# Optimization experiments

Measured on AMD Instinct MI355X. Metric: run time of the kernel, lower is better.

The kernel has to match this reference:

```python
import jax, jax.numpy as jnp
import numpy as np

N = 50000
E = 800000
EQ = 200000
IN_DIM = 256
H1 = 256
H2 = 128
EA = 16


def _lrelu(x):
    return jax.nn.leaky_relu(x, negative_slope=0.01)


def gcn_conv(h, edge_index, W, b, num_nodes):
    # PyG GCNConv: add self-loops, symmetric normalization, out = A_hat (h W) + b
    row, col = edge_index[0], edge_index[1]
    loop = jnp.arange(num_nodes, dtype=row.dtype)
    row = jnp.concatenate([row, loop])
    col = jnp.concatenate([col, loop])
    deg = jax.ops.segment_sum(jnp.ones(row.shape[0], dtype=h.dtype), col, num_segments=num_nodes)
    dinv = jnp.where(deg > 0, jax.lax.rsqrt(deg), 0.0)
    norm = dinv[row] * dinv[col]                      # [E+N]
    hw = h @ W                                        # [N, out]
    msg = hw[row] * norm[:, None]                     # gather + scale
    out = jax.ops.segment_sum(msg, col, num_segments=num_nodes)
    return out + b


def gru_cell(x, h, Wih, Whh, bih, bhh):
    # torch.nn.GRUCell, gate order (r, z, n); Wih/Whh stored as [in, 3H]
    gi = x @ Wih + bih
    gh = h @ Whh + bhh
    ir, iz, inn = jnp.split(gi, 3, axis=1)
    hr, hz, hn = jnp.split(gh, 3, axis=1)
    r = jax.nn.sigmoid(ir + hr)
    z = jax.nn.sigmoid(iz + hz)
    n = jnp.tanh(inn + r * hn)
    return (1.0 - z) * n + z * h


def setup_inputs() -> dict:
    key = jax.random.key(0)
    ks = jax.random.split(key, 24)

    def gn(k, shape, scale=0.05):
        return (jax.random.normal(k, shape, dtype=jnp.float32) * scale)

    inp = {
        "x": jax.random.normal(ks[0], (N, IN_DIM), dtype=jnp.float32),
        "edge_index": jax.random.randint(ks[1], (2, E), 0, N, dtype=jnp.int32).astype(jnp.int64),
        "edge_label_index": jax.random.randint(ks[2], (2, EQ), 0, N, dtype=jnp.int32).astype(jnp.int64),
        "edge_attr": jax.random.normal(ks[3], (EQ, EA), dtype=jnp.float32),
        "prev1": jax.random.normal(ks[4], (N, H1), dtype=jnp.float32) * 0.1,
        "prev2": jax.random.normal(ks[5], (N, H2), dtype=jnp.float32) * 0.1,
        "pre1_W": gn(ks[6], (IN_DIM, 256)), "pre1_b": jnp.zeros((256,), jnp.float32),
        "pre2_W": gn(ks[7], (256, 128)), "pre2_b": jnp.zeros((128,), jnp.float32),
        "conv1_W": gn(ks[8], (128, H1)), "conv1_b": jnp.zeros((H1,), jnp.float32),
        "conv2_W": gn(ks[9], (H1, H2)), "conv2_b": jnp.zeros((H2,), jnp.float32),
        "gru1_Wih": gn(ks[10], (H1, 3 * H1)), "gru1_Whh": gn(ks[11], (H1, 3 * H1)),
        "gru1_bih": jnp.zeros((3 * H1,), jnp.float32), "gru1_bhh": jnp.zeros((3 * H1,), jnp.float32),
        "gru2_Wih": gn(ks[12], (H2, 3 * H2)), "gru2_Whh": gn(ks[13], (H2, 3 * H2)),
        "gru2_bih": jnp.zeros((3 * H2,), jnp.float32), "gru2_bhh": jnp.zeros((3 * H2,), jnp.float32),
        "post_W": gn(ks[14], (2 * H2 + EA, 1)), "post_b": jnp.zeros((1,), jnp.float32),
    }
    return inp


def reference(x, edge_index, edge_label_index, edge_attr, prev1, prev2,
              pre1_W, pre1_b, pre2_W, pre2_b,
              conv1_W, conv1_b, conv2_W, conv2_b,
              gru1_Wih, gru1_Whh, gru1_bih, gru1_bhh,
              gru2_Wih, gru2_Whh, gru2_bih, gru2_bhh,
              post_W, post_b):
    num_nodes = x.shape[0]
    # dense preprocessing (dropout p=0.0 -> identity)
    h = _lrelu(x @ pre1_W + pre1_b)
    h = _lrelu(h @ pre2_W + pre2_b)          # [N,128]
    # GCN layer 1 + GRU update with previous embeddings
    h = _lrelu(gcn_conv(h, edge_index, conv1_W, conv1_b, num_nodes))
    h = gru_cell(h, prev1, gru1_Wih, gru1_Whh, gru1_bih, gru1_bhh)
    emb1 = h
    # GCN layer 2 + GRU update
    h = _lrelu(gcn_conv(h, edge_index, conv2_W, conv2_b, num_nodes))
    h = gru_cell(h, prev2, gru2_Wih, gru2_Whh, gru2_bih, gru2_bhh)
    emb2 = h
    # edge-level prediction: gather endpoints, concat with edge_attr, linear
    h_src = h[edge_label_index[0]]
    h_dst = h[edge_label_index[1]]
    combined = jnp.concatenate([h_src, h_dst, edge_attr], axis=1)  # [Eq, 2*H2+EA]
    scores = (combined @ post_W + post_b).reshape(-1)              # [Eq]
    return (scores, emb1, emb2)
```

## Files before the change

### kernel.cpp

```cpp
#include <hip/hip_runtime.h>
#include <hip/hip_bf16.h>

#define DEVFN __device__ __forceinline__

constexpr int NN = 50000;
constexpr int NE = 800000;
constexpr int NQ = 200000;
constexpr long MP = 50048;

typedef __attribute__((ext_vector_type(8))) short bf16x8;
typedef __attribute__((ext_vector_type(2))) short s16x2;
typedef __attribute__((ext_vector_type(4))) float f32x4;
typedef __attribute__((address_space(1))) const void gv_t;
typedef __attribute__((address_space(3))) void lv_t;

DEVFN float lrelu(float x) { return x > 0.f ? x : 0.01f * x; }
DEVFN float sigmoidf(float x) { return 1.f / (1.f + __expf(-x)); }

DEVFN short f2b(float v) {
    __hip_bfloat16 h = __float2bfloat16(v);
    return *reinterpret_cast<short*>(&h);
}
DEVFN float b2f(short s) {
    union { unsigned u; float f; } z;
    z.u = ((unsigned)(unsigned short)s) << 16;
    return z.f;
}
DEVFN void gld16(const void* g, void* l) {
    __builtin_amdgcn_global_load_lds((gv_t*)g, (lv_t*)l, 16, 0, 0);
}

DEVFN void swz_rc(int d, int nwg, int NC, int& rw, int& cs) {
    int q0 = nwg >> 3, rr = nwg & 7;
    int xcd = d & 7, idx = d >> 3;
    int w = (xcd < rr ? xcd * (q0 + 1) : rr * (q0 + 1) + (xcd - rr) * q0) + idx;
    rw = w / NC;
    cs = w - rw * NC;
}

template <int H>
DEVFN float gruw_val(const float* Wih, const float* Whh, int i) {
    constexpr int K2 = 2 * H, W3 = 3 * H;
    int np = i / K2, k = i % K2;
    int g16 = np >> 6, chunk = (np >> 4) & 3, cl = np & 15;
    int c = g16 * 16 + cl;
    if (chunk == 0) return (k < H) ? Wih[(long)k * W3 + c] : Whh[(long)(k - H) * W3 + c];
    if (chunk == 1) return (k < H) ? Wih[(long)k * W3 + H + c] : Whh[(long)(k - H) * W3 + H + c];
    if (chunk == 2) return (k < H) ? Wih[(long)k * W3 + 2 * H + c] : 0.f;
    return (k < H) ? 0.f : Whh[(long)(k - H) * W3 + 2 * H + c];
}

__global__ void prep_all(const float* __restrict__ x, const float* __restrict__ prev1,
                         const float* __restrict__ pre1W, const float* __restrict__ pre2W,
                         const float* __restrict__ conv1W, const float* __restrict__ conv2W,
                         const float* __restrict__ g1ih, const float* __restrict__ g1hh,
                         const float* __restrict__ g2ih, const float* __restrict__ g2hh,
                         short* __restrict__ xb, short* __restrict__ AP1,
                         short* __restrict__ pre1T, short* __restrict__ pre2T,
                         short* __restrict__ conv1T, short* __restrict__ conv2T,
                         short* __restrict__ W1g1, short* __restrict__ W1g2) {
    long i = (long)blockIdx.x * 256 + threadIdx.x;
    if (i < MP * 256) {
        xb[i] = (i < (long)NN * 256) ? f2b(x[i]) : (short)0;
        return;
    }
    i -= MP * 256;
    if (i < (long)NN * 256) {
        long r = i >> 8; int c = (int)(i & 255);
        AP1[r * 512 + 256 + c] = f2b(prev1[i]);
        return;
    }
    i -= (long)NN * 256;
    if (i < 65536) { int ii = (int)i, n = ii >> 8, k = ii & 255; pre1T[ii] = f2b(pre1W[k * 256 + n]); return; }
    i -= 65536;
    if (i < 32768) { int ii = (int)i, n = ii >> 8, k = ii & 255; pre2T[ii] = f2b(pre2W[k * 128 + n]); return; }
    i -= 32768;
    if (i < 32768) { int ii = (int)i, n = ii >> 7, k = ii & 127; conv1T[ii] = f2b(conv1W[k * 256 + n]); return; }
    i -= 32768;
    if (i < 32768) { int ii = (int)i, n = ii >> 8, k = ii & 255; conv2T[ii] = f2b(conv2W[k * 128 + n]); return; }
    i -= 32768;
    if (i < 524288) { W1g1[i] = f2b(gruw_val<256>(g1ih, g1hh, (int)i)); return; }
    i -= 524288;
    if (i < 131072) W1g2[i] = f2b(gruw_val<128>(g2ih, g2hh, (int)i));
}

__global__ void f2b_strided(const float* __restrict__ in, short* __restrict__ out,
                            int H, long n) {
    long i = (long)blockIdx.x * 256 + threadIdx.x;
    if (i >= n) return;
    long r = i / H;
    int c = i % H;
    out[r * 2 * H + H + c] = f2b(in[i]);
}

template <int EPI>
__global__ __launch_bounds__(256)
void gemm_mfma(const short* __restrict__ A, const short* __restrict__ Bt,
               const float* __restrict__ bias,
               short* __restrict__ Cb, int K, int obS, int NC, int nwg) {
    __shared__ alignas(16) short As[2][4096];
    __shared__ alignas(16) short Bs[2][4096];
    const int tid = threadIdx.x;
    const int lane = tid & 63, w = tid >> 6;
    const int wr = w >> 1, wc = w & 1;
    int rw, cs;
    swz_rc(blockIdx.x, nwg, NC, rw, cs);
    const long row0 = (long)rw * 128;
    const long col0 = (long)cs * 128;

    f32x4 acc[4][4] = {};

    const int kcs = ((tid & 3) ^ ((tid >> 3) & 3)) * 8;
    const short* gA = A + (row0 + (tid >> 2)) * (long)K + kcs;
    const short* gB = Bt + (col0 + (tid >> 2)) * (long)K + kcs;
    const long half = 64 * (long)K;

    auto stage = [&](int b, int k0) {
        gld16(gA + k0, &As[b][tid * 8]);
        gld16(gA + half + k0, &As[b][2048 + tid * 8]);
        gld16(gB + k0, &Bs[b][tid * 8]);
        gld16(gB + half + k0, &Bs[b][2048 + tid * 8]);
    };

    stage(0, 0);
    int cur = 0;
    const int l15 = lane & 15;
    const int kq = ((lane >> 4) ^ ((l15 >> 1) & 3)) * 8;
    for (int k0 = 0; k0 < K; k0 += 32) {
        __syncthreads();
        if (k0 + 32 < K) stage(cur ^ 1, k0 + 32);
        bf16x8 af[4], bfr[4];
#pragma unroll
        for (int i = 0; i < 4; ++i)
            af[i] = *(const bf16x8*)&As[cur][(wr * 64 + i * 16 + l15) * 32 + kq];
#pragma unroll
        for (int j = 0; j < 4; ++j)
            bfr[j] = *(const bf16x8*)&Bs[cur][(wc * 64 + j * 16 + l15) * 32 + kq];
#pragma unroll
        for (int i = 0; i < 4; ++i)
#pragma unroll
            for (int j = 0; j < 4; ++j)
                acc[i][j] = __builtin_amdgcn_mfma_f32_16x16x32_bf16(af[i], bfr[j], acc[i][j], 0, 0, 0);
        cur ^= 1;
    }

    const int cr = (lane >> 4) * 4, cc = lane & 15;
#pragma unroll
    for (int i = 0; i < 4; ++i) {
#pragma unroll
        for (int j = 0; j < 4; ++j) {
            const long col = col0 + wc * 64 + j * 16 + cc;
            float bv = (EPI == 1) ? bias[col] : 0.f;
#pragma unroll
            for (int r = 0; r < 4; ++r) {
                const long row = row0 + wr * 64 + i * 16 + cr + r;
                float v = acc[i][j][r];
                if (EPI == 1) v = lrelu(v + bv);
                Cb[row * obS + col] = f2b(v);
            }
        }
    }
}

template <int H, bool WRITEB>
__global__ __launch_bounds__(256)
void gru_wide(const short* __restrict__ AP, const short* __restrict__ W1,
              const float* __restrict__ prevf,
              const float* __restrict__ bih, const float* __restrict__ bhh,
              float* __restrict__ outF, short* __restrict__ outB, int M,
              int NC, int nwg) {
    constexpr int K2 = 2 * H;
    __shared__ alignas(16) short As[2][4096];
    __shared__ alignas(16) short Bs[2][4096];
    const int tid = threadIdx.x;
    const int lane = tid & 63, w = tid >> 6;
    const int wr = w >> 1, wc = w & 1;
    int rw, cs;
    swz_rc(blockIdx.x, nwg, NC, rw, cs);
    const long row0 = (long)rw * 128;
    const long col0 = (long)cs * 128;

    f32x4 acc[4][4] = {};

    const int kcs = ((tid & 3) ^ ((tid >> 3) & 3)) * 8;
    const short* gA = AP + (row0 + (tid >> 2)) * (long)K2 + kcs;
    const short* gB = W1 + (col0 + (tid >> 2)) * (long)K2 + kcs;
    const long half = 64 * (long)K2;

    auto stage = [&](int b, int k0) {
        const bool lo = (k0 < H);
        gld16(gA + k0, &As[b][tid * 8]);
        gld16(gA + half + k0, &As[b][2048 + tid * 8]);
        const bool bskip = (w == 2 && !lo) || (w == 3 && lo);
        if (!bskip) {
            gld16(gB + k0, &Bs[b][tid * 8]);
            gld16(gB + half + k0, &Bs[b][2048 + tid * 8]);
        }
    };

    stage(0, 0);
    int cur = 0;
    const int l15 = lane & 15;
    const int kq = ((lane >> 4) ^ ((l15 >> 1) & 3)) * 8;
    for (int k0 = 0; k0 < K2; k0 += 32) {
        const bool lo = (k0 < H);
        __syncthreads();
        if (k0 + 32 < K2) stage(cur ^ 1, k0 + 32);
        bf16x8 af[4], bfr[4];
#pragma unroll
        for (int i = 0; i < 4; ++i)
            af[i] = *(const bf16x8*)&As[cur][(wr * 64 + i * 16 + l15) * 32 + kq];
#pragma unroll
        for (int j = 0; j < 4; ++j) {
            if ((j == 2 && !lo) || (j == 3 && lo)) continue;
            bfr[j] = *(const bf16x8*)&Bs[cur][(wc * 64 + j * 16 + l15) * 32 + kq];
        }
#pragma unroll
        for (int i = 0; i < 4; ++i)
#pragma unroll
            for (int j = 0; j < 4; ++j) {
                if ((j == 2 && !lo) || (j == 3 && lo)) continue;
                acc[i][j] = __builtin_amdgcn_mfma_f32_16x16x32_bf16(af[i], bfr[j], acc[i][j], 0, 0, 0);
            }
        cur ^= 1;
    }

    const int cr = (lane >> 4) * 4;
    const int c = cs * 32 + wc * 16 + (lane & 15);
    const float bsr = bih[c] + bhh[c];
    const float bsz = bih[H + c] + bhh[H + c];
    const float bin = bih[2 * H + c];
    const float bhn = bhh[2 * H + c];
#pragma unroll
    for (int i = 0; i < 4; ++i) {
#pragma unroll
        for (int r = 0; r < 4; ++r) {
            const long row = row0 + wr * 64 + i * 16 + cr + r;
            if (row >= M) continue;
            float rg = sigmoidf(acc[i][0][r] + bsr);
            float zg = sigmoidf(acc[i][1][r] + bsz);
            float ng = tanhf(acc[i][2][r] + bin + rg * (acc[i][3][r] + bhn));
            float o = (1.f - zg) * ng + zg * prevf[row * (long)H + c];
            outF[row * (long)H + c] = o;
            if (WRITEB) outB[row * (long)H + c] = f2b(o);
        }
    }
}

__global__ void cnt_kernel(const int* __restrict__ cols, int* __restrict__ cnt, int E) {
    int e = blockIdx.x * 256 + threadIdx.x;
    if (e < E) atomicAdd(&cnt[cols[e]], 1);
}

__global__ void scan1(const int* __restrict__ cnt, int* __restrict__ off,
                      int* __restrict__ bsum, float* __restrict__ dinv, int n) {
    __shared__ int sm[256];
    int i = blockIdx.x * 256 + threadIdx.x;
    int v = (i < n) ? cnt[i] : 0;
    if (i < n) dinv[i] = rsqrtf((float)v + 1.0f);
    sm[threadIdx.x] = v;
    __syncthreads();
    for (int s = 1; s < 256; s <<= 1) {
        int t = (threadIdx.x >= s) ? sm[threadIdx.x - s] : 0;
        __syncthreads();
        sm[threadIdx.x] += t;
        __syncthreads();
    }
    if (i < n) off[i + 1] = sm[threadIdx.x];
    if (threadIdx.x == 255) bsum[blockIdx.x] = sm[255];
}

__global__ void scan2(int* __restrict__ bsum, int nb) {
    __shared__ int sm[256];
    int v = (threadIdx.x < nb) ? bsum[threadIdx.x] : 0;
    sm[threadIdx.x] = v;
    __syncthreads();
    for (int s = 1; s < 256; s <<= 1) {
        int t = (threadIdx.x >= s) ? sm[threadIdx.x - s] : 0;
        __syncthreads();
        sm[threadIdx.x] += t;
        __syncthreads();
    }
    if (threadIdx.x < nb) bsum[threadIdx.x] = sm[threadIdx.x] - v;
}

__global__ void scan3(int* __restrict__ off, const int* __restrict__ bsum, int n) {
    int i = blockIdx.x * 256 + threadIdx.x;
    if (i < n) off[i + 1] += bsum[blockIdx.x];
    if (i == 0) off[0] = 0;
}

__global__ void fill_csr(const int* __restrict__ rows, const int* __restrict__ cols,
                         const float* __restrict__ dinv, const int* __restrict__ off,
                         int* __restrict__ cursor, int* __restrict__ srow,
                         float* __restrict__ snorm, int E) {
    int e = blockIdx.x * 256 + threadIdx.x;
    if (e >= E) return;
    int r = rows[e], c = cols[e];
    int p = off[c] + atomicAdd(&cursor[c], 1);
    srow[p] = r;
    snorm[p] = dinv[r] * dinv[c];
}

template <int OS, bool EPI>
__global__ __launch_bounds__(256)
void gather_agg(const short* __restrict__ hwb, const int* __restrict__ off,
                const int* __restrict__ srow, const float* __restrict__ snorm,
                const float* __restrict__ dinv, const float* __restrict__ bias,
                short* __restrict__ aggb, int n) {
    constexpr int H = 128;
    int t = blockIdx.x * 256 + threadIdx.x;
    int c = t >> 6, l = t & 63;
    if (c >= n) return;
    const int fo = l * 2;
    float acc0, acc1;
    {
        float dd = dinv[c] * dinv[c];
        s16x2 v = *(const s16x2*)&hwb[(long)c * H + fo];
        acc0 = b2f(v[0]) * dd;
        acc1 = b2f(v[1]) * dd;
    }
    int e = off[c];
    const int e1 = off[c + 1];
    for (; e + 3 < e1; e += 4) {
        int r0 = srow[e], r1 = srow[e + 1], r2 = srow[e + 2], r3 = srow[e + 3];
        float n0 = snorm[e], n1 = snorm[e + 1], n2 = snorm[e + 2], n3 = snorm[e + 3];
        s16x2 v0 = *(const s16x2*)&hwb[(long)r0 * H + fo];
        s16x2 v1 = *(const s16x2*)&hwb[(long)r1 * H + fo];
        s16x2 v2 = *(const s16x2*)&hwb[(long)r2 * H + fo];
        s16x2 v3 = *(const s16x2*)&hwb[(long)r3 * H + fo];
        acc0 += b2f(v0[0]) * n0 + b2f(v1[0]) * n1 + b2f(v2[0]) * n2 + b2f(v3[0]) * n3;
        acc1 += b2f(v0[1]) * n0 + b2f(v1[1]) * n1 + b2f(v2[1]) * n2 + b2f(v3[1]) * n3;
    }
    for (; e < e1; ++e) {
        int r0 = srow[e];
        float n0 = snorm[e];
        s16x2 v0 = *(const s16x2*)&hwb[(long)r0 * H + fo];
        acc0 += b2f(v0[0]) * n0;
        acc1 += b2f(v0[1]) * n0;
    }
    s16x2 o;
    if (EPI) {
        o[0] = f2b(lrelu(acc0 + bias[fo]));
        o[1] = f2b(lrelu(acc1 + bias[fo + 1]));
    } else {
        o[0] = f2b(acc0);
        o[1] = f2b(acc1);
    }
    *(s16x2*)&aggb[(long)c * OS + fo] = o;
}

__global__ void edge_score_b(const short* __restrict__ emb2b, const int* __restrict__ eli,
                             const float* __restrict__ ea, const float* __restrict__ pw,
                             const float* __restrict__ pb, float* __restrict__ scores, int Q) {
    int t = blockIdx.x * 256 + threadIdx.x;
    int e = t >> 6, l = t & 63;
    if (e >= Q) return;
    int s = eli[e], d = eli[Q + e];
    const int f = l * 2;
    s16x2 vs = *(const s16x2*)&emb2b[(long)s * 128 + f];
    s16x2 vd = *(const s16x2*)&emb2b[(long)d * 128 + f];
    float acc = b2f(vs[0]) * pw[f] + b2f(vs[1]) * pw[f + 1]
              + b2f(vd[0]) * pw[128 + f] + b2f(vd[1]) * pw[128 + f + 1];
    if (l < 16) acc += ea[(long)e * 16 + l] * pw[256 + l];
#pragma unroll
    for (int off = 32; off > 0; off >>= 1) acc += __shfl_down(acc, off);
    if (l == 0) scores[e] = acc + pb[0];
}


extern "C" void kernel_launch(void* const* d_in, const int* in_sizes, int n_in,
                              void* d_out, int out_size, void* d_ws, size_t ws_size,
                              hipStream_t stream) {
    const float* x       = (const float*)d_in[0];
    const int*   ei      = (const int*)d_in[1];
    const int*   eli     = (const int*)d_in[2];
    const float* eattr   = (const float*)d_in[3];
    const float* prev1   = (const float*)d_in[4];
    const float* prev2   = (const float*)d_in[5];
    const float* pre1_W  = (const float*)d_in[6];
    const float* pre1_b  = (const float*)d_in[7];
    const float* pre2_W  = (const float*)d_in[8];
    const float* pre2_b  = (const float*)d_in[9];
    const float* conv1_W = (const float*)d_in[10];
    const float* conv1_b = (const float*)d_in[11];
    const float* conv2_W = (const float*)d_in[12];
    const float* conv2_b = (const float*)d_in[13];
    const float* g1_Wih  = (const float*)d_in[14];
    const float* g1_Whh  = (const float*)d_in[15];
    const float* g1_bih  = (const float*)d_in[16];
    const float* g1_bhh  = (const float*)d_in[17];
    const float* g2_Wih  = (const float*)d_in[18];
    const float* g2_Whh  = (const float*)d_in[19];
    const float* g2_bih  = (const float*)d_in[20];
    const float* g2_bhh  = (const float*)d_in[21];
    const float* post_W  = (const float*)d_in[22];
    const float* post_b  = (const float*)d_in[23];

    float* out    = (float*)d_out;
    float* scores = out;
    float* emb1   = out + NQ;
    float* emb2   = emb1 + (long)NN * 256;

    char* ws = (char*)d_ws;
    const long S256 = MP * 256 * 2;
    const long S128 = MP * 128 * 2;
    short* R1  = (short*)ws;
    short* R2  = (short*)(ws + S256);
    short* R3  = (short*)(ws + 2 * S256);
    short* AP1 = (short*)(ws + 2 * S256 + S128);
    short* AP2 = R1;
    char*  wts = ws + 4 * S256 + S128;
    short* pre1T  = (short*)wts;
    short* pre2T  = pre1T + 256 * 256;
    short* conv1T = pre2T + 128 * 256;
    short* conv2T = conv1T + 256 * 128;
    short* W1g1   = conv2T + 128 * 256;
    short* W1g2   = W1g1 + 1024 * 512;
    float* dinv   = (float*)(W1g2 + 512 * 256);
    int*   cnt    = (int*)(dinv + NN);
    int*   cursor = cnt + NN;
    int*   off    = cursor + NN;
    int*   bsum   = off + NN + 1;
    int*   srow   = bsum + 256;
    float* snorm  = (float*)(srow + NE);

    const int* rows = ei;
    const int* cols = ei + NE;

    dim3 blk(256);
    const int NB = (NN + 255) / 256;

    const long PREP = MP * 256 + (long)NN * 256 + 65536 + 3 * 32768 + 524288 + 131072;
    prep_all<<<(int)((PREP + 255) / 256), blk, 0, stream>>>(
        x, prev1, pre1_W, pre2_W, conv1_W, conv2_W,
        g1_Wih, g1_Whh, g2_Wih, g2_Whh,
        R1, AP1, pre1T, pre2T, conv1T, conv2T, W1g1, W1g2);

    hipMemsetAsync(cnt, 0, 2 * NN * sizeof(int), stream);
    cnt_kernel<<<(NE + 255) / 256, blk, 0, stream>>>(cols, cnt, NE);
    scan1<<<NB, blk, 0, stream>>>(cnt, off, bsum, dinv, NN);
    scan2<<<1, blk, 0, stream>>>(bsum, NB);
    scan3<<<NB, blk, 0, stream>>>(off, bsum, NN);
    fill_csr<<<(NE + 255) / 256, blk, 0, stream>>>(rows, cols, dinv, off, cursor, srow, snorm, NE);

    gemm_mfma<1><<<782, blk, 0, stream>>>(R1, pre1T, pre1_b, R2, 256, 256, 2, 782);
    gemm_mfma<1><<<391, blk, 0, stream>>>(R2, pre2T, pre2_b, R3, 256, 128, 1, 391);

    gather_agg<128, false><<<(NN + 3) / 4, blk, 0, stream>>>(R3, off, srow, snorm, dinv, nullptr, R1, NN);
    gemm_mfma<1><<<782, blk, 0, stream>>>(R1, conv1T, conv1_b, AP1, 128, 512, 2, 782);

    gru_wide<256, true><<<3128, blk, 0, stream>>>(AP1, W1g1, prev1, g1_bih, g1_bhh,
                                                  emb1, R2, NN, 8, 3128);

    f2b_strided<<<(int)(((long)NN * 128 + 255) / 256), blk, 0, stream>>>(prev2, AP2, 128, (long)NN * 128);

    gemm_mfma<0><<<391, blk, 0, stream>>>(R2, conv2T, nullptr, R3, 256, 128, 1, 391);

    gather_agg<256, true><<<(NN + 3) / 4, blk, 0, stream>>>(R3, off, srow, snorm, dinv, conv2_b, AP2, NN);

    gru_wide<128, true><<<1564, blk, 0, stream>>>(AP2, W1g2, prev2, g2_bih, g2_bhh,
                                                  emb2, R3, NN, 4, 1564);

    edge_score_b<<<NQ / 4, blk, 0, stream>>>(R3, eli, eattr, post_W, post_b, scores, NQ);
}
```

Baseline: 480.9 us.

## Triple-buffer GEMM stages, fuse prev2 conversion into gather, use fast tanh

The MFMA GEMM and GRU kernels move from a double buffer to a fully unrolled triple-buffered LDS pipeline, using explicit vmcnt waits and raw barriers so that two stages of loads are in flight. The separate f2b_strided launch is dropped and the prev2 bf16 conversion is folded into the second gather_agg kernel. tanhf in the GRU epilogue becomes an exp-based fast tanh, and the GRU B-loads no longer skip the unused quarter tiles. The extra LDS buffer lowers occupancy, the loads that were skipped are now fetched, and the fast tanh is slightly less accurate.

```diff
diff --git a/kernel.cpp b/kernel.cpp
--- a/kernel.cpp
+++ b/kernel.cpp
@@ -10,12 +10,18 @@
 
 typedef __attribute__((ext_vector_type(8))) short bf16x8;
 typedef __attribute__((ext_vector_type(2))) short s16x2;
+typedef __attribute__((ext_vector_type(2))) float f32x2;
 typedef __attribute__((ext_vector_type(4))) float f32x4;
 typedef __attribute__((address_space(1))) const void gv_t;
 typedef __attribute__((address_space(3))) void lv_t;
 
 DEVFN float lrelu(float x) { return x > 0.f ? x : 0.01f * x; }
 DEVFN float sigmoidf(float x) { return 1.f / (1.f + __expf(-x)); }
+DEVFN float tanh_fast(float x) {
+    float xc = fminf(fmaxf(x, -15.f), 15.f);
+    float t = __expf(2.f * xc);
+    return (t - 1.f) / (t + 1.f);
+}
 
 DEVFN short f2b(float v) {
     __hip_bfloat16 h = __float2bfloat16(v);
@@ -29,6 +35,10 @@
 DEVFN void gld16(const void* g, void* l) {
     __builtin_amdgcn_global_load_lds((gv_t*)g, (lv_t*)l, 16, 0, 0);
 }
+
+#define WAITV4 asm volatile("s_waitcnt vmcnt(4)" ::: "memory")
+#define WAITV0 asm volatile("s_waitcnt vmcnt(0)" ::: "memory")
+#define CFENCE asm volatile("" ::: "memory")
 
 DEVFN void swz_rc(int d, int nwg, int NC, int& rw, int& cs) {
     int q0 = nwg >> 3, rr = nwg & 7;
@@ -84,22 +94,14 @@
     if (i < 131072) W1g2[i] = f2b(gruw_val<128>(g2ih, g2hh, (int)i));
 }
 
-__global__ void f2b_strided(const float* __restrict__ in, short* __restrict__ out,
-                            int H, long n) {
-    long i = (long)blockIdx.x * 256 + threadIdx.x;
-    if (i >= n) return;
-    long r = i / H;
-    int c = i % H;
-    out[r * 2 * H + H + c] = f2b(in[i]);
-}
-
-template <int EPI>
+template <int EPI, int K>
 __global__ __launch_bounds__(256)
 void gemm_mfma(const short* __restrict__ A, const short* __restrict__ Bt,
                const float* __restrict__ bias,
-               short* __restrict__ Cb, int K, int obS, int NC, int nwg) {
-    __shared__ alignas(16) short As[2][4096];
-    __shared__ alignas(16) short Bs[2][4096];
+               short* __restrict__ Cb, int obS, int NC, int nwg) {
+    constexpr int NS = K / 32;
+    __shared__ alignas(16) short As[3][4096];
+    __shared__ alignas(16) short Bs[3][4096];
     const int tid = threadIdx.x;
     const int lane = tid & 63, w = tid >> 6;
     const int wr = w >> 1, wc = w & 1;
@@ -123,12 +125,16 @@
     };
 
     stage(0, 0);
-    int cur = 0;
+    stage(1, 32);
     const int l15 = lane & 15;
     const int kq = ((lane >> 4) ^ ((l15 >> 1) & 3)) * 8;
-    for (int k0 = 0; k0 < K; k0 += 32) {
-        __syncthreads();
-        if (k0 + 32 < K) stage(cur ^ 1, k0 + 32);
+#pragma unroll
+    for (int t = 0; t < NS; ++t) {
+        if (t + 1 < NS) { WAITV4; } else { WAITV0; }
+        __builtin_amdgcn_s_barrier();
+        CFENCE;
+        if (t + 2 < NS) stage((t + 2) % 3, (t + 2) * 32);
+        const int cur = t % 3;
         bf16x8 af[4], bfr[4];
 #pragma unroll
         for (int i = 0; i < 4; ++i)
@@ -141,7 +147,6 @@
 #pragma unroll
             for (int j = 0; j < 4; ++j)
                 acc[i][j] = __builtin_amdgcn_mfma_f32_16x16x32_bf16(af[i], bfr[j], acc[i][j], 0, 0, 0);
-        cur ^= 1;
     }
 
     const int cr = (lane >> 4) * 4, cc = lane & 15;
@@ -170,42 +175,42 @@
               float* __restrict__ outF, short* __restrict__ outB, int M,
               int NC, int nwg) {
     constexpr int K2 = 2 * H;
-    __shared__ alignas(16) short As[2][4096];
-    __shared__ alignas(16) short Bs[2][4096];
+    constexpr int NS = K2 / 32;
+    __shared__ alignas(16) short As[3][4096];
+    __shared__ alignas(16) short Bs[3][4096];
     const int tid = threadIdx.x;
     const int lane = tid & 63, w = tid >> 6;
     const int wr = w >> 1, wc = w & 1;
     int rw, cs;
     swz_rc(blockIdx.x, nwg, NC, rw, cs);
     const long row0 = (long)rw * 128;
-    const long col0 = (long)cs * 128;
 
     f32x4 acc[4][4] = {};
 
     const int kcs = ((tid & 3) ^ ((tid >> 3) & 3)) * 8;
     const short* gA = AP + (row0 + (tid >> 2)) * (long)K2 + kcs;
-    const short* gB = W1 + (col0 + (tid >> 2)) * (long)K2 + kcs;
+    const short* gB = W1 + ((long)cs * 128 + (tid >> 2)) * (long)K2 + kcs;
     const long half = 64 * (long)K2;
 
     auto stage = [&](int b, int k0) {
-        const bool lo = (k0 < H);
         gld16(gA + k0, &As[b][tid * 8]);
         gld16(gA + half + k0, &As[b][2048 + tid * 8]);
-        const bool bskip = (w == 2 && !lo) || (w == 3 && lo);
-        if (!bskip) {
-            gld16(gB + k0, &Bs[b][tid * 8]);
-            gld16(gB + half + k0, &Bs[b][2048 + tid * 8]);
-        }
+        gld16(gB + k0, &Bs[b][tid * 8]);
+        gld16(gB + half + k0, &Bs[b][2048 + tid * 8]);
     };
 
     stage(0, 0);
-    int cur = 0;
+    stage(1, 32);
     const int l15 = lane & 15;
     const int kq = ((lane >> 4) ^ ((l15 >> 1) & 3)) * 8;
-    for (int k0 = 0; k0 < K2; k0 += 32) {
-        const bool lo = (k0 < H);
-        __syncthreads();
-        if (k0 + 32 < K2) stage(cur ^ 1, k0 + 32);
+#pragma unroll
+    for (int t = 0; t < NS; ++t) {
+        const bool lo = (t * 32 < H);
+        if (t + 1 < NS) { WAITV4; } else { WAITV0; }
+        __builtin_amdgcn_s_barrier();
+        CFENCE;
+        if (t + 2 < NS) stage((t + 2) % 3, (t + 2) * 32);
+        const int cur = t % 3;
         bf16x8 af[4], bfr[4];
 #pragma unroll
         for (int i = 0; i < 4; ++i)
@@ -222,7 +227,6 @@
                 if ((j == 2 && !lo) || (j == 3 && lo)) continue;
                 acc[i][j] = __builtin_amdgcn_mfma_f32_16x16x32_bf16(af[i], bfr[j], acc[i][j], 0, 0, 0);
             }
-        cur ^= 1;
     }
 
     const int cr = (lane >> 4) * 4;
@@ -239,7 +243,7 @@
             if (row >= M) continue;
             float rg = sigmoidf(acc[i][0][r] + bsr);
             float zg = sigmoidf(acc[i][1][r] + bsz);
-            float ng = tanhf(acc[i][2][r] + bin + rg * (acc[i][3][r] + bhn));
+            float ng = tanh_fast(acc[i][2][r] + bin + rg * (acc[i][3][r] + bhn));
             float o = (1.f - zg) * ng + zg * prevf[row * (long)H + c];
             outF[row * (long)H + c] = o;
             if (WRITEB) outB[row * (long)H + c] = f2b(o);
@@ -302,11 +306,12 @@
     snorm[p] = dinv[r] * dinv[c];
 }
 
-template <int OS, bool EPI>
+template <int OS, bool EPI, bool PREV>
 __global__ __launch_bounds__(256)
 void gather_agg(const short* __restrict__ hwb, const int* __restrict__ off,
                 const int* __restrict__ srow, const float* __restrict__ snorm,
                 const float* __restrict__ dinv, const float* __restrict__ bias,
+                const float* __restrict__ prevf,
                 short* __restrict__ aggb, int n) {
     constexpr int H = 128;
     int t = blockIdx.x * 256 + threadIdx.x;
@@ -348,6 +353,13 @@
         o[1] = f2b(acc1);
     }
     *(s16x2*)&aggb[(long)c * OS + fo] = o;
+    if (PREV) {
+        f32x2 p = *(const f32x2*)&prevf[(long)c * H + fo];
+        s16x2 pb;
+        pb[0] = f2b(p[0]);
+        pb[1] = f2b(p[1]);
+        *(s16x2*)&aggb[(long)c * OS + H + fo] = pb;
+    }
 }
 
 __global__ void edge_score_b(const short* __restrict__ emb2b, const int* __restrict__ eli,
@@ -444,20 +456,20 @@
     scan3<<<NB, blk, 0, stream>>>(off, bsum, NN);
     fill_csr<<<(NE + 255) / 256, blk, 0, stream>>>(rows, cols, dinv, off, cursor, srow, snorm, NE);
 
-    gemm_mfma<1><<<782, blk, 0, stream>>>(R1, pre1T, pre1_b, R2, 256, 256, 2, 782);
-    gemm_mfma<1><<<391, blk, 0, stream>>>(R2, pre2T, pre2_b, R3, 256, 128, 1, 391);
-
-    gather_agg<128, false><<<(NN + 3) / 4, blk, 0, stream>>>(R3, off, srow, snorm, dinv, nullptr, R1, NN);
-    gemm_mfma<1><<<782, blk, 0, stream>>>(R1, conv1T, conv1_b, AP1, 128, 512, 2, 782);
+    gemm_mfma<1, 256><<<782, blk, 0, stream>>>(R1, pre1T, pre1_b, R2, 256, 2, 782);
+    gemm_mfma<1, 256><<<391, blk, 0, stream>>>(R2, pre2T, pre2_b, R3, 128, 1, 391);
+
+    gather_agg<128, false, false><<<(NN + 3) / 4, blk, 0, stream>>>(
+        R3, off, srow, snorm, dinv, nullptr, nullptr, R1, NN);
+    gemm_mfma<1, 128><<<782, blk, 0, stream>>>(R1, conv1T, conv1_b, AP1, 512, 2, 782);
 
     gru_wide<256, true><<<3128, blk, 0, stream>>>(AP1, W1g1, prev1, g1_bih, g1_bhh,
                                                   emb1, R2, NN, 8, 3128);
 
-    f2b_strided<<<(int)(((long)NN * 128 + 255) / 256), blk, 0, stream>>>(prev2, AP2, 128, (long)NN * 128);
-
-    gemm_mfma<0><<<391, blk, 0, stream>>>(R2, conv2T, nullptr, R3, 256, 128, 1, 391);
-
-    gather_agg<256, true><<<(NN + 3) / 4, blk, 0, stream>>>(R3, off, srow, snorm, dinv, conv2_b, AP2, NN);
+    gemm_mfma<0, 256><<<391, blk, 0, stream>>>(R2, conv2T, nullptr, R3, 128, 1, 391);
+
+    gather_agg<256, true, true><<<(NN + 3) / 4, blk, 0, stream>>>(
+        R3, off, srow, snorm, dinv, conv2_b, prev2, AP2, NN);
 
     gru_wide<128, true><<<1564, blk, 0, stream>>>(AP2, W1g2, prev2, g2_bih, g2_bhh,
                                                   emb2, R3, NN, 4, 1564);
```

Result: faster. 459.3 us (-4.5%).
